# Kernel tuning notes

Hardware: AMD Instinct MI355X
Metric: run time of the kernel (lower is better)

The kernel has to match this reference:

```python
import jax, jax.numpy as jnp
import numpy as np

B, S, H, NH = 4, 1024, 2048, 32
HD = H // NH
EPS = 1e-5

def layer_norm(x, w, b):
    mu = jnp.mean(x, axis=-1, keepdims=True)
    var = jnp.mean(jnp.square(x - mu), axis=-1, keepdims=True)
    return (x - mu) * jax.lax.rsqrt(var + EPS) * w + b

def setup_inputs() -> dict:
    key = jax.random.key(0)
    ks = jax.random.split(key, 8)
    s = 0.02
    inp = {
        'hidden_states': jax.random.normal(ks[0], (B, S, H), jnp.float32),
        'mask': jnp.tril(jnp.ones((S, S), jnp.float32))[None, None],  # causal 0/1
        'ln1_w': jnp.ones((H,), jnp.float32), 'ln1_b': jnp.zeros((H,), jnp.float32),
        'w_qkv': s * jax.random.normal(ks[1], (H, 3 * H), jnp.float32),
        'b_qkv': jnp.zeros((3 * H,), jnp.float32),
        'w_dense': s * jax.random.normal(ks[2], (H, H), jnp.float32),
        'b_dense': jnp.zeros((H,), jnp.float32),
        'ln3_w': jnp.ones((H,), jnp.float32), 'ln3_b': jnp.zeros((H,), jnp.float32),
        'ln2_w': jnp.ones((H,), jnp.float32), 'ln2_b': jnp.zeros((H,), jnp.float32),
        'w_h4h': s * jax.random.normal(ks[3], (H, 4 * H), jnp.float32),
        'b_h4h': jnp.zeros((4 * H,), jnp.float32),
        'w_4hh': s * jax.random.normal(ks[4], (4 * H, H), jnp.float32),
        'b_4hh': jnp.zeros((H,), jnp.float32),
        'ln4_w': jnp.ones((H,), jnp.float32), 'ln4_b': jnp.zeros((H,), jnp.float32),
    }
    return inp

def _layer(hidden_states, mask, ln1_w, ln1_b, w_qkv, b_qkv, w_dense, b_dense,
           ln3_w, ln3_b, ln2_w, ln2_b, w_h4h, b_h4h, w_4hh, b_4hh, ln4_w, ln4_b):
    # --- input LN ---
    x1 = layer_norm(hidden_states, ln1_w, ln1_b)
    # --- self attention ---
    qkv = x1 @ w_qkv + b_qkv                              # [B,S,3H]
    q, k, v = jnp.split(qkv, 3, axis=-1)
    def heads(t):  # [B,S,H] -> [B,NH,S,HD]
        return t.reshape(B, S, NH, HD).transpose(0, 2, 1, 3)
    q, k, v = heads(q), heads(k), heads(v)
    scores = jnp.einsum('bnqd,bnkd->bnqk', q / jnp.sqrt(jnp.float32(HD)), k)
    scores = scores * mask - 10000.0 * (1.0 - mask)
    probs = jax.nn.softmax(scores, axis=-1)
    ctx = jnp.einsum('bnqk,bnkd->bnqd', probs, v)
    ctx = ctx.transpose(0, 2, 1, 3).reshape(B, S, H)
    attn_out = ctx @ w_dense + b_dense
    # sandwich LN on attention output
    attn_out = layer_norm(attn_out, ln3_w, ln3_b)
    ln_input = hidden_states + attn_out
    # --- MLP ---
    x2 = layer_norm(ln_input, ln2_w, ln2_b)
    inter = jax.nn.gelu(x2 @ w_h4h + b_h4h, approximate=True)
    mlp_out = inter @ w_4hh + b_4hh
    mlp_out = layer_norm(mlp_out, ln4_w, ln4_b)
    return ln_input + mlp_out

def reference(hidden_states, mask, ln1_w, ln1_b, w_qkv, b_qkv, w_dense, b_dense,
              ln3_w, ln3_b, ln2_w, ln2_b, w_h4h, b_h4h, w_4hh, b_4hh, ln4_w, ln4_b):
    return _layer(hidden_states, mask, ln1_w, ln1_b, w_qkv, b_qkv, w_dense, b_dense,
                  ln3_w, ln3_b, ln2_w, ln2_b, w_h4h, b_h4h, w_4hh, b_4hh, ln4_w, ln4_b)
```

## Files before the change

### kernel.cpp

```cpp
#include <hip/hip_runtime.h>
#include <cstdint>
#include <cstddef>

typedef __bf16 bf16_t;
typedef __bf16 bf16x8 __attribute__((ext_vector_type(8)));
typedef float f32x4 __attribute__((ext_vector_type(4)));

#define BB 4
#define SS 1024
#define HH 2048
#define NHH 32
#define HDD 64
#define MTOK 4096
#define QKVLD 6144

static constexpr size_t OFF_WQKV   = 0;
static constexpr size_t OFF_WDENSE = 25165824;
static constexpr size_t OFF_WH4H   = 33554432;
static constexpr size_t OFF_W4HH   = 67108864;
static constexpr size_t OFF_X1     = 100663296;
static constexpr size_t OFF_QKV    = 117440512;
static constexpr size_t OFF_ATTND2 = 150994944;
static constexpr size_t OFF_VT     = 167772160;
static constexpr size_t OFF_LNIN   = 184549376;
static constexpr size_t OFF_MLP    = 218103808;
static constexpr size_t OFF_MLP2   = 234881024;

__device__ __forceinline__ uint16_t f2bfu(float f) {
  union { float f; uint32_t u; } v; v.f = f;
  return (uint16_t)((v.u + 0x7FFFu + ((v.u >> 16) & 1u)) >> 16);
}
__device__ __forceinline__ bf16_t f2bf(float f) {
  union { uint16_t u; bf16_t b; } o; o.u = f2bfu(f);
  return o.b;
}
__device__ __forceinline__ float bfu2f(uint16_t u) {
  union { uint32_t u; float f; } v; v.u = ((uint32_t)u) << 16;
  return v.f;
}

__device__ __forceinline__ void g2l16(const void* g, void* l) {
  __builtin_amdgcn_global_load_lds(
      (const __attribute__((address_space(1))) void*)g,
      (__attribute__((address_space(3))) void*)l, 16, 0, 0);
}

__global__ void convert_all_kernel(const float* __restrict__ w0, bf16_t* __restrict__ o0,
                                   const float* __restrict__ w1, bf16_t* __restrict__ o1,
                                   const float* __restrict__ w2, bf16_t* __restrict__ o2,
                                   const float* __restrict__ w3, bf16_t* __restrict__ o3) {
  __shared__ float t[32][33];
  int id = blockIdx.x;
  const float* W; bf16_t* WT; int K, N, nt, idx;
  if (id < 12288)      { W = w0; WT = o0; K = 2048; N = 6144; nt = 192; idx = id; }
  else if (id < 16384) { W = w1; WT = o1; K = 2048; N = 2048; nt = 64;  idx = id - 12288; }
  else if (id < 32768) { W = w2; WT = o2; K = 2048; N = 8192; nt = 256; idx = id - 16384; }
  else                 { W = w3; WT = o3; K = 8192; N = 2048; nt = 64;  idx = id - 32768; }
  const int n0 = (idx % nt) * 32;
  const int k0 = (idx / nt) * 32;
  const int tx = threadIdx.x, ty = threadIdx.y;
#pragma unroll
  for (int j = 0; j < 4; ++j)
    t[ty + j * 8][tx] = W[(size_t)(k0 + ty + j * 8) * N + n0 + tx];
  __syncthreads();
#pragma unroll
  for (int j = 0; j < 4; ++j)
    WT[(size_t)(n0 + ty + j * 8) * K + k0 + tx] = f2bf(t[tx][ty + j * 8]);
}

__global__ void transpose_v_kernel(const bf16_t* __restrict__ qkv, bf16_t* __restrict__ vT) {
  __shared__ bf16_t t[32][33];
  const int s0 = blockIdx.x * 32;
  const int d0 = blockIdx.y * 32;
  const int bh = blockIdx.z;
  const int b = bh >> 5, h = bh & 31;
  const int tx = threadIdx.x, ty = threadIdx.y;
  const bf16_t* src = qkv + (size_t)b * SS * QKVLD + 2 * HH + h * HDD;
#pragma unroll
  for (int j = 0; j < 4; ++j)
    t[ty + j * 8][tx] = src[(size_t)(s0 + ty + j * 8) * QKVLD + d0 + tx];
  __syncthreads();
  bf16_t* dst = vT + (size_t)bh * HDD * SS;
#pragma unroll
  for (int j = 0; j < 4; ++j)
    dst[(size_t)(d0 + ty + j * 8) * SS + s0 + tx] = t[tx][ty + j * 8];
}

__device__ __forceinline__ void block_reduce2(float& s, float& ss) {
#pragma unroll
  for (int o = 32; o > 0; o >>= 1) {
    s += __shfl_down(s, o, 64);
    ss += __shfl_down(ss, o, 64);
  }
  __shared__ float red[8];
  const int wave = threadIdx.x >> 6;
  const int lane = threadIdx.x & 63;
  if (lane == 0) { red[wave] = s; red[4 + wave] = ss; }
  __syncthreads();
  s = red[0] + red[1] + red[2] + red[3];
  ss = red[4] + red[5] + red[6] + red[7];
  __syncthreads();
}

__device__ __forceinline__ void load8(const float* base, int tid, float* v) {
  float4 a = ((const float4*)base)[tid];
  float4 b = ((const float4*)base)[tid + 256];
  v[0] = a.x; v[1] = a.y; v[2] = a.z; v[3] = a.w;
  v[4] = b.x; v[5] = b.y; v[6] = b.z; v[7] = b.w;
}
__device__ __forceinline__ void load8bf(const bf16_t* base, int tid, float* v) {
  ushort4 a = ((const ushort4*)base)[tid];
  ushort4 b = ((const ushort4*)base)[tid + 256];
  v[0] = bfu2f(a.x); v[1] = bfu2f(a.y); v[2] = bfu2f(a.z); v[3] = bfu2f(a.w);
  v[4] = bfu2f(b.x); v[5] = bfu2f(b.y); v[6] = bfu2f(b.z); v[7] = bfu2f(b.w);
}
__device__ __forceinline__ void store8f(float* base, int tid, const float* v) {
  ((float4*)base)[tid] = make_float4(v[0], v[1], v[2], v[3]);
  ((float4*)base)[tid + 256] = make_float4(v[4], v[5], v[6], v[7]);
}
__device__ __forceinline__ void store8bf(bf16_t* base, int tid, const float* v) {
  ushort4 o0 = {f2bfu(v[0]), f2bfu(v[1]), f2bfu(v[2]), f2bfu(v[3])};
  ushort4 o1 = {f2bfu(v[4]), f2bfu(v[5]), f2bfu(v[6]), f2bfu(v[7])};
  ((ushort4*)base)[tid] = o0;
  ((ushort4*)base)[tid + 256] = o1;
}
__device__ __forceinline__ void row_stats(const float* v, float& mean, float& inv) {
  float s = 0.f, ss = 0.f;
#pragma unroll
  for (int i = 0; i < 8; ++i) { s += v[i]; ss += v[i] * v[i]; }
  block_reduce2(s, ss);
  mean = s * (1.0f / 2048.0f);
  float var = ss * (1.0f / 2048.0f) - mean * mean;
  inv = rsqrtf(var + 1e-5f);
}

__global__ __launch_bounds__(256) void ln1_kernel(const float* __restrict__ x,
                                                  const float* __restrict__ w,
                                                  const float* __restrict__ b,
                                                  bf16_t* __restrict__ out) {
  const int row = blockIdx.x, tid = threadIdx.x;
  float v[8], wv[8], bv[8], o[8];
  load8(x + (size_t)row * HH, tid, v);
  float mean, inv;
  row_stats(v, mean, inv);
  load8(w, tid, wv);
  load8(b, tid, bv);
#pragma unroll
  for (int i = 0; i < 8; ++i) o[i] = (v[i] - mean) * inv * wv[i] + bv[i];
  store8bf(out + (size_t)row * HH, tid, o);
}

__global__ __launch_bounds__(256) void fuse_mid_kernel(
    const bf16_t* __restrict__ ad, const bf16_t* __restrict__ ad2,
    const float* __restrict__ hid,
    const float* __restrict__ w3, const float* __restrict__ b3,
    const float* __restrict__ w2, const float* __restrict__ b2,
    float* __restrict__ lnin, bf16_t* __restrict__ x2) {
  const int row = blockIdx.x, tid = threadIdx.x;
  float a[8], a2[8], h[8], wv[8], bv[8], l[8], o[8];
  load8bf(ad + (size_t)row * HH, tid, a);
  load8bf(ad2 + (size_t)row * HH, tid, a2);
#pragma unroll
  for (int i = 0; i < 8; ++i) a[i] += a2[i];
  float mean3, inv3;
  row_stats(a, mean3, inv3);
  load8(hid + (size_t)row * HH, tid, h);
  load8(w3, tid, wv);
  load8(b3, tid, bv);
#pragma unroll
  for (int i = 0; i < 8; ++i) l[i] = h[i] + (a[i] - mean3) * inv3 * wv[i] + bv[i];
  store8f(lnin + (size_t)row * HH, tid, l);
  float mean2, inv2;
  row_stats(l, mean2, inv2);
  load8(w2, tid, wv);
  load8(b2, tid, bv);
#pragma unroll
  for (int i = 0; i < 8; ++i) o[i] = (l[i] - mean2) * inv2 * wv[i] + bv[i];
  store8bf(x2 + (size_t)row * HH, tid, o);
}

__global__ __launch_bounds__(256) void fuse_out_kernel(
    const bf16_t* __restrict__ mlp, const bf16_t* __restrict__ mlp2,
    const float* __restrict__ lnin,
    const float* __restrict__ w4, const float* __restrict__ b4,
    float* __restrict__ out) {
  const int row = blockIdx.x, tid = threadIdx.x;
  float m[8], m2[8], l[8], wv[8], bv[8], o[8];
  load8bf(mlp + (size_t)row * HH, tid, m);
  load8bf(mlp2 + (size_t)row * HH, tid, m2);
#pragma unroll
  for (int i = 0; i < 8; ++i) m[i] += m2[i];
  float mean4, inv4;
  row_stats(m, mean4, inv4);
  load8(lnin + (size_t)row * HH, tid, l);
  load8(w4, tid, wv);
  load8(b4, tid, bv);
#pragma unroll
  for (int i = 0; i < 8; ++i) o[i] = l[i] + (m[i] - mean4) * inv4 * wv[i] + bv[i];
  store8f(out + (size_t)row * HH, tid, o);
}

#define MFMA16(a, b, cc) __builtin_amdgcn_mfma_f32_16x16x32_bf16(a, b, cc, 0, 0, 0)

#define STAGE(ISB, BUF, HALF, KT) do {                                              \
    const char* _s = ((ISB) ? bS : aS) + (size_t)(HALF) * h128 + (size_t)(KT) * 128; \
    char* _d = lds + ((ISB) ? 65536 : 0) + (BUF) * 32768 + (HALF) * 16384 +         \
               wave * 1024;                                                         \
    g2l16(_s, _d);                                                                  \
    g2l16(_s + h64, _d + 8192);                                                     \
  } while (0)

#define LDA(BUF, MQ)                                                                \
  _Pragma("unroll") for (int mf = 0; mf < 4; ++mf) {                                \
    const char* _p = aRd + (BUF) * 32768 + (MQ) * 8192 + mf * 2048;                 \
    aR[mf * 2]     = *(const bf16x8*)(_p + colK0);                                  \
    aR[mf * 2 + 1] = *(const bf16x8*)(_p + colK1);                                  \
  }

#define LDB(BR, BUF, NQ)                                                            \
  _Pragma("unroll") for (int nf = 0; nf < 2; ++nf) {                                \
    const char* _p = bRd + (BUF) * 32768 + (NQ) * 4096 + nf * 2048;                 \
    BR[nf * 2]     = *(const bf16x8*)(_p + colK0);                                  \
    BR[nf * 2 + 1] = *(const bf16x8*)(_p + colK1);                                  \
  }

#define MMA(MQ, NQ, BR)                                                             \
  _Pragma("unroll") for (int mf = 0; mf < 4; ++mf)                                  \
  _Pragma("unroll") for (int nf = 0; nf < 2; ++nf)                                  \
  _Pragma("unroll") for (int ks = 0; ks < 2; ++ks)                                  \
    acc[(MQ) * 4 + mf][(NQ) * 2 + nf] =                                             \
        MFMA16(aR[mf * 2 + ks], BR[nf * 2 + ks], acc[(MQ) * 4 + mf][(NQ) * 2 + nf]);

#define BARS()                                                                      \
  __builtin_amdgcn_sched_barrier(0);                                                \
  __builtin_amdgcn_s_barrier();                                                     \
  asm volatile("s_waitcnt lgkmcnt(0)" ::: "memory");                                \
  __builtin_amdgcn_sched_barrier(0);                                                \
  __builtin_amdgcn_s_setprio(1);

#define ENDP()                                                                      \
  __builtin_amdgcn_s_setprio(0);                                                    \
  __builtin_amdgcn_sched_barrier(0);                                                \
  __builtin_amdgcn_s_barrier();

template <int EPI, int SPLITK>
__global__ __launch_bounds__(512, 2) void gemm256(
    const bf16_t* __restrict__ A, const bf16_t* __restrict__ BT,
    const float* __restrict__ bias, void* __restrict__ out0, void* __restrict__ out1,
    const int M, const int N, const int Keff, const int ldK) {
  __shared__ alignas(16) char lds[131072];
  const int tid = threadIdx.x;
  const int wave = tid >> 6, lane = tid & 63;
  const int wm = wave >> 2, wn = wave & 3;
  const int c = lane & 15, g = lane >> 4;

  const int nwg = gridDim.x;
  int bid = (blockIdx.x & 7) * (nwg >> 3) + (blockIdx.x >> 3);
  const int nm = M >> 8;
  int slice = 0;
  if (SPLITK == 2) {
    const int per = nm * (N >> 8);
    slice = bid >= per;
    bid -= slice * per;
  }
  const int mt = bid % nm, nt = bid / nm;

  const size_t ldb = (size_t)ldK * 2;
  const size_t h64 = (size_t)64 * ldb;
  const size_t h128 = 2 * h64;
  const char* aPan = (const char*)A + (size_t)(mt * 256) * ldb + (size_t)(slice * Keff) * 2;
  const char* bPan = (const char*)BT + (size_t)(nt * 256) * ldb + (size_t)(slice * Keff) * 2;

  const int srow = tid >> 3;
  const int scb = ((tid & 7) << 4) ^ ((srow & 7) << 4);
  const char* aS = aPan + (size_t)srow * ldb + scb;
  const char* bS = bPan + (size_t)srow * ldb + scb;

  const int x4 = (c & 7) << 4;
  const int colK0 = (g * 16) ^ x4;
  const int colK1 = (64 + g * 16) ^ x4;
  const char* aRd = lds + wm * 16384 + c * 128;
  const char* bRd = lds + 65536 + (wn >> 1) * 16384 + ((wn & 1) * 64 + c) * 128;

  f32x4 acc[8][4] = {};
  bf16x8 aR[8], b0R[4], b1R[4];

  const int NITER = Keff >> 7;
  const int NT2 = NITER * 2;

  STAGE(1, 0, 0, 0); STAGE(1, 0, 1, 0); STAGE(0, 0, 0, 0); STAGE(0, 0, 1, 0);
  STAGE(1, 1, 0, 1); STAGE(1, 1, 1, 1);
  asm volatile("s_waitcnt vmcnt(4)" ::: "memory");
  __builtin_amdgcn_s_barrier();

  for (int it = 0; it < NITER; ++it) {
    const int ktb = 2 * it + 1;
    int kt2 = 2 * it + 2; if (kt2 >= NT2) kt2 = 0;
    int kt3 = 2 * it + 3; if (kt3 >= NT2) kt3 = 0;
    LDA(0, 0); LDB(b0R, 0, 0); STAGE(0, 1, 0, ktb);
    BARS(); MMA(0, 0, b0R); ENDP();
    LDB(b1R, 0, 1); STAGE(0, 1, 1, ktb);
    BARS(); MMA(0, 1, b1R); ENDP();
    LDA(0, 1); STAGE(1, 0, 0, kt2);
    BARS(); MMA(1, 1, b1R); ENDP();
    STAGE(1, 0, 1, kt2);
    asm volatile("s_waitcnt vmcnt(4)" ::: "memory");
    BARS(); MMA(1, 0, b0R); ENDP();
    LDA(1, 0); LDB(b0R, 1, 0); STAGE(0, 0, 0, kt2);
    BARS(); MMA(0, 0, b0R); ENDP();
    LDB(b1R, 1, 1); STAGE(0, 0, 1, kt2);
    BARS(); MMA(0, 1, b1R); ENDP();
    LDA(1, 1); STAGE(1, 1, 0, kt3);
    BARS(); MMA(1, 1, b1R); ENDP();
    STAGE(1, 1, 1, kt3);
    asm volatile("s_waitcnt vmcnt(4)" ::: "memory");
    BARS(); MMA(1, 0, b0R); ENDP();
  }

  const int rowb = mt * 256 + wm * 128 + g * 4;
  const int colb = nt * 256 + wn * 64 + c;
  if constexpr (EPI == 0) {
    bf16_t* o = (bf16_t*)(slice ? out1 : out0);
    float bvv[4];
#pragma unroll
    for (int nf = 0; nf < 4; ++nf) bvv[nf] = (slice == 0) ? bias[colb + nf * 16] : 0.0f;
#pragma unroll
    for (int mf = 0; mf < 8; ++mf) {
      const int r = rowb + mf * 16;
#pragma unroll
      for (int e = 0; e < 4; ++e) {
        bf16_t* orow = o + (size_t)(r + e) * N + colb;
#pragma unroll
        for (int nf = 0; nf < 4; ++nf)
          orow[nf * 16] = f2bf(acc[mf][nf][e] + bvv[nf]);
      }
    }
  } else if constexpr (EPI == 1) {
    bf16_t* o = (bf16_t*)out0;
    float bvv[4];
#pragma unroll
    for (int nf = 0; nf < 4; ++nf) bvv[nf] = bias[colb + nf * 16];
#pragma unroll
    for (int mf = 0; mf < 8; ++mf) {
      const int r = rowb + mf * 16;
#pragma unroll
      for (int e = 0; e < 4; ++e) {
        bf16_t* orow = o + (size_t)(r + e) * N + colb;
#pragma unroll
        for (int nf = 0; nf < 4; ++nf)
          orow[nf * 16] = f2bf(acc[mf][nf][e] + bvv[nf]);
      }
    }
  } else {
    bf16_t* o = (bf16_t*)out0;
    float bvv[4];
#pragma unroll
    for (int nf = 0; nf < 4; ++nf) bvv[nf] = bias[colb + nf * 16];
#pragma unroll
    for (int mf = 0; mf < 8; ++mf) {
      const int r = rowb + mf * 16;
#pragma unroll
      for (int e = 0; e < 4; ++e) {
        bf16_t* orow = o + (size_t)(r + e) * N + colb;
#pragma unroll
        for (int nf = 0; nf < 4; ++nf) {
          float u = acc[mf][nf][e] + bvv[nf];
          float cc2 = 0.7978845608f * (u + 0.044715f * u * u * u);
          float ex = __expf(2.0f * cc2);
          float th = 1.0f - 2.0f / (ex + 1.0f);
          orow[nf * 16] = f2bf(0.5f * u * (1.0f + th));
        }
      }
    }
  }
}

__global__ __launch_bounds__(512) void attn_kernel(
    const bf16_t* __restrict__ qkv, const bf16_t* __restrict__ vT,
    bf16_t* __restrict__ ctx) {
  __shared__ alignas(16) char Ksm[8192];
  __shared__ alignas(16) char Vsm[8192];
  __shared__ alignas(16) char Psm[16384];

  const int id = blockIdx.x;
  const int qt = 7 - (id >> 7);
  const int bh = id & 127;
  const int b = bh >> 5, h = bh & 31;
  const int tid = threadIdx.x;
  const int wave = tid >> 6;
  const int lane = tid & 63;
  const int q0 = qt * 128;
  const int q0w = q0 + wave * 16;
  const int c = lane & 15;
  const int g = lane >> 4;

  const bf16_t* qb = qkv + ((size_t)b * SS + q0w) * QKVLD + h * HDD;
  const bf16x8 qa0 = *(const bf16x8*)(qb + (size_t)c * QKVLD + g * 8);
  const bf16x8 qa1 = *(const bf16x8*)(qb + (size_t)c * QKVLD + 32 + g * 8);

  f32x4 o[4] = {};
  float mrow[4], lrow[4];
#pragma unroll
  for (int e = 0; e < 4; ++e) { mrow[e] = -1e30f; lrow[e] = 0.0f; }

  const int sr = tid >> 3;
  const int sgb = ((tid & 7) * 16) ^ ((sr & 7) << 4);
  const char* kgb = (const char*)(qkv + (size_t)b * SS * QKVLD + HH + h * HDD);
  const char* vgb = (const char*)(vT + (size_t)bh * HDD * SS);
  char* kdst = Ksm + wave * 1024;
  char* vdst = Vsm + wave * 1024;
  char* Pw = Psm + wave * 2048;

  const int ntiles = (q0 + 128) >> 6;

  for (int t = 0; t < ntiles; ++t) {
    const int kb = t * 64;
    g2l16(kgb + (size_t)(kb + sr) * (QKVLD * 2) + sgb, kdst);
    g2l16(vgb + (size_t)sr * 2048 + (size_t)kb * 2 + sgb, vdst);
    __syncthreads();

    if (kb < q0w + 16) {
      f32x4 s[4] = {};
#pragma unroll
      for (int sub = 0; sub < 4; ++sub) {
        const int n = sub * 16 + c;
        const int x = (n & 7) << 4;
        bf16x8 kf0 = *(const bf16x8*)(Ksm + n * 128 + ((g * 16) ^ x));
        bf16x8 kf1 = *(const bf16x8*)(Ksm + n * 128 + ((64 + g * 16) ^ x));
        s[sub] = MFMA16(qa0, kf0, s[sub]);
        s[sub] = MFMA16(qa1, kf1, s[sub]);
      }
      const bool diag = (kb + 63 > q0w);
      float pv[4][4];
#pragma unroll
      for (int sub = 0; sub < 4; ++sub)
#pragma unroll
        for (int e = 0; e < 4; ++e) {
          float sv = s[sub][e] * 0.125f;
          if (diag && (kb + sub * 16 + c > q0w + g * 4 + e)) sv = -10000.0f;
          pv[sub][e] = sv;
        }
      float scale[4];
#pragma unroll
      for (int e = 0; e < 4; ++e) {
        float mx = fmaxf(fmaxf(pv[0][e], pv[1][e]), fmaxf(pv[2][e], pv[3][e]));
        mx = fmaxf(mx, __shfl_xor(mx, 1, 64));
        mx = fmaxf(mx, __shfl_xor(mx, 2, 64));
        mx = fmaxf(mx, __shfl_xor(mx, 4, 64));
        mx = fmaxf(mx, __shfl_xor(mx, 8, 64));
        const float mnew = fmaxf(mrow[e], mx);
        scale[e] = __expf(mrow[e] - mnew);
        mrow[e] = mnew;
      }
#pragma unroll
      for (int e = 0; e < 4; ++e) {
        const int row = g * 4 + e;
        const int xr = (row & 7) << 4;
        float sum = 0.0f;
#pragma unroll
        for (int sub = 0; sub < 4; ++sub) {
          float p = __expf(pv[sub][e] - mrow[e]);
          sum += p;
          const int cb = (sub * 16 + c) * 2;
          *(bf16_t*)(Pw + row * 128 + (cb ^ xr)) = f2bf(p);
        }
        sum += __shfl_xor(sum, 1, 64);
        sum += __shfl_xor(sum, 2, 64);
        sum += __shfl_xor(sum, 4, 64);
        sum += __shfl_xor(sum, 8, 64);
        lrow[e] = lrow[e] * scale[e] + sum;
      }
#pragma unroll
      for (int d = 0; d < 4; ++d)
#pragma unroll
        for (int e = 0; e < 4; ++e) o[d][e] *= scale[e];
      const int xa = (c & 7) << 4;
      bf16x8 pa0 = *(const bf16x8*)(Pw + c * 128 + ((g * 16) ^ xa));
      bf16x8 pa1 = *(const bf16x8*)(Pw + c * 128 + ((64 + g * 16) ^ xa));
#pragma unroll
      for (int d = 0; d < 4; ++d) {
        const int n = d * 16 + c;
        const int xv = (n & 7) << 4;
        bf16x8 vf0 = *(const bf16x8*)(Vsm + n * 128 + ((g * 16) ^ xv));
        bf16x8 vf1 = *(const bf16x8*)(Vsm + n * 128 + ((64 + g * 16) ^ xv));
        o[d] = MFMA16(pa0, vf0, o[d]);
        o[d] = MFMA16(pa1, vf1, o[d]);
      }
    }
    __syncthreads();
  }

#pragma unroll
  for (int e = 0; e < 4; ++e) {
    const int qrow = q0w + g * 4 + e;
    const float inv = 1.0f / lrow[e];
#pragma unroll
    for (int d = 0; d < 4; ++d)
      ctx[((size_t)b * SS + qrow) * HH + h * 64 + d * 16 + c] = f2bf(o[d][e] * inv);
  }
}

extern "C" void kernel_launch(void* const* d_in, const int* in_sizes, int n_in,
                              void* d_out, int out_size, void* d_ws, size_t ws_size,
                              hipStream_t stream) {
  const float* hidden = (const float*)d_in[0];
  const float* ln1w = (const float*)d_in[2];
  const float* ln1b = (const float*)d_in[3];
  const float* wqkv = (const float*)d_in[4];
  const float* bqkv = (const float*)d_in[5];
  const float* wdense = (const float*)d_in[6];
  const float* bdense = (const float*)d_in[7];
  const float* ln3w = (const float*)d_in[8];
  const float* ln3b = (const float*)d_in[9];
  const float* ln2w = (const float*)d_in[10];
  const float* ln2b = (const float*)d_in[11];
  const float* wh4h = (const float*)d_in[12];
  const float* bh4h = (const float*)d_in[13];
  const float* w4hh = (const float*)d_in[14];
  const float* b4hh = (const float*)d_in[15];
  const float* ln4w = (const float*)d_in[16];
  const float* ln4b = (const float*)d_in[17];

  char* ws = (char*)d_ws;
  bf16_t* wqkvT = (bf16_t*)(ws + OFF_WQKV);
  bf16_t* wdenseT = (bf16_t*)(ws + OFF_WDENSE);
  bf16_t* wh4hT = (bf16_t*)(ws + OFF_WH4H);
  bf16_t* w4hhT = (bf16_t*)(ws + OFF_W4HH);
  bf16_t* x1 = (bf16_t*)(ws + OFF_X1);
  bf16_t* qkv = (bf16_t*)(ws + OFF_QKV);
  bf16_t* vT = (bf16_t*)(ws + OFF_VT);
  bf16_t* ctx = (bf16_t*)(ws + OFF_X1);
  bf16_t* attnd = (bf16_t*)(ws + OFF_QKV);
  bf16_t* attnd2 = (bf16_t*)(ws + OFF_ATTND2);
  float* lnin = (float*)(ws + OFF_LNIN);
  bf16_t* x2 = (bf16_t*)(ws + OFF_X1);
  bf16_t* inter = (bf16_t*)(ws + OFF_QKV);
  bf16_t* mlp = (bf16_t*)(ws + OFF_MLP);
  bf16_t* mlp2 = (bf16_t*)(ws + OFF_MLP2);

  dim3 tb(32, 8);
  convert_all_kernel<<<dim3(49152), tb, 0, stream>>>(wqkv, wqkvT, wdense, wdenseT,
                                                     wh4h, wh4hT, w4hh, w4hhT);

  ln1_kernel<<<MTOK, 256, 0, stream>>>(hidden, ln1w, ln1b, x1);

  gemm256<1, 1><<<dim3((6144 / 256) * (4096 / 256)), 512, 0, stream>>>(
      x1, wqkvT, bqkv, (void*)qkv, nullptr, MTOK, 6144, 2048, 2048);

  transpose_v_kernel<<<dim3(SS / 32, HDD / 32, BB * NHH), tb, 0, stream>>>(qkv, vT);

  attn_kernel<<<dim3(1024), 512, 0, stream>>>(qkv, vT, ctx);

  gemm256<0, 2><<<dim3((2048 / 256) * (4096 / 256) * 2), 512, 0, stream>>>(
      ctx, wdenseT, bdense, (void*)attnd, (void*)attnd2, MTOK, 2048, 1024, 2048);

  fuse_mid_kernel<<<MTOK, 256, 0, stream>>>(attnd, attnd2, hidden, ln3w, ln3b, ln2w, ln2b, lnin, x2);

  gemm256<2, 1><<<dim3((8192 / 256) * (4096 / 256)), 512, 0, stream>>>(
      x2, wh4hT, bh4h, (void*)inter, nullptr, MTOK, 8192, 2048, 2048);

  gemm256<0, 2><<<dim3((2048 / 256) * (4096 / 256) * 2), 512, 0, stream>>>(
      inter, w4hhT, b4hh, (void*)mlp, (void*)mlp2, MTOK, 2048, 4096, 8192);

  fuse_out_kernel<<<MTOK, 256, 0, stream>>>(mlp, mlp2, lnin, ln4w, ln4b, (float*)d_out);
}
```

Baseline: 594.3 us.

## Software-pipeline LDS fragment loads behind MFMA phases in GEMM main loop

Restructures the 256x256 GEMM K-loop so that the LDS-to-register fragment loads for the next phase are issued after the current phase's MFMAs, between the priority drop and the closing barrier. A prologue load before the loop and a final load at the end of each iteration keep the pipeline primed. The explicit lgkmcnt(0) waits and sched_barrier fences are removed, leaving wait placement and interleaving to the compiler. The goal is to hide LDS read latency under matrix-core work. The cost is more live fragment registers and reliance on the compiler to order LDS reads correctly against the async global-to-LDS staging.

```diff
diff --git a/kernel.cpp b/kernel.cpp
--- a/kernel.cpp
+++ b/kernel.cpp
@@ -231,16 +231,14 @@
     acc[(MQ) * 4 + mf][(NQ) * 2 + nf] =                                             \
         MFMA16(aR[mf * 2 + ks], BR[nf * 2 + ks], acc[(MQ) * 4 + mf][(NQ) * 2 + nf]);
 
-#define BARS()                                                                      \
-  __builtin_amdgcn_sched_barrier(0);                                                \
+#define PH_BEGIN()                                                                  \
   __builtin_amdgcn_s_barrier();                                                     \
-  asm volatile("s_waitcnt lgkmcnt(0)" ::: "memory");                                \
-  __builtin_amdgcn_sched_barrier(0);                                                \
   __builtin_amdgcn_s_setprio(1);
 
-#define ENDP()                                                                      \
-  __builtin_amdgcn_s_setprio(0);                                                    \
-  __builtin_amdgcn_sched_barrier(0);                                                \
+#define PH_MID()                                                                    \
+  __builtin_amdgcn_s_setprio(0);
+
+#define PH_END()                                                                    \
   __builtin_amdgcn_s_barrier();
 
 template <int EPI, int SPLITK>
@@ -292,29 +290,45 @@
   STAGE(1, 1, 0, 1); STAGE(1, 1, 1, 1);
   asm volatile("s_waitcnt vmcnt(4)" ::: "memory");
   __builtin_amdgcn_s_barrier();
+  LDA(0, 0);
+  LDB(b0R, 0, 0);
 
   for (int it = 0; it < NITER; ++it) {
     const int ktb = 2 * it + 1;
     int kt2 = 2 * it + 2; if (kt2 >= NT2) kt2 = 0;
     int kt3 = 2 * it + 3; if (kt3 >= NT2) kt3 = 0;
-    LDA(0, 0); LDB(b0R, 0, 0); STAGE(0, 1, 0, ktb);
-    BARS(); MMA(0, 0, b0R); ENDP();
-    LDB(b1R, 0, 1); STAGE(0, 1, 1, ktb);
-    BARS(); MMA(0, 1, b1R); ENDP();
-    LDA(0, 1); STAGE(1, 0, 0, kt2);
-    BARS(); MMA(1, 1, b1R); ENDP();
+    STAGE(0, 1, 0, ktb);
+    PH_BEGIN(); MMA(0, 0, b0R); PH_MID();
+    LDB(b1R, 0, 1);
+    PH_END();
+    STAGE(0, 1, 1, ktb);
+    PH_BEGIN(); MMA(0, 1, b1R); PH_MID();
+    LDA(0, 1);
+    PH_END();
+    STAGE(1, 0, 0, kt2);
+    PH_BEGIN(); MMA(1, 1, b1R); PH_MID();
+    PH_END();
     STAGE(1, 0, 1, kt2);
     asm volatile("s_waitcnt vmcnt(4)" ::: "memory");
-    BARS(); MMA(1, 0, b0R); ENDP();
-    LDA(1, 0); LDB(b0R, 1, 0); STAGE(0, 0, 0, kt2);
-    BARS(); MMA(0, 0, b0R); ENDP();
-    LDB(b1R, 1, 1); STAGE(0, 0, 1, kt2);
-    BARS(); MMA(0, 1, b1R); ENDP();
-    LDA(1, 1); STAGE(1, 1, 0, kt3);
-    BARS(); MMA(1, 1, b1R); ENDP();
+    PH_BEGIN(); MMA(1, 0, b0R); PH_MID();
+    LDA(1, 0); LDB(b0R, 1, 0);
+    PH_END();
+    STAGE(0, 0, 0, kt2);
+    PH_BEGIN(); MMA(0, 0, b0R); PH_MID();
+    LDB(b1R, 1, 1);
+    PH_END();
+    STAGE(0, 0, 1, kt2);
+    PH_BEGIN(); MMA(0, 1, b1R); PH_MID();
+    LDA(1, 1);
+    PH_END();
+    STAGE(1, 1, 0, kt3);
+    PH_BEGIN(); MMA(1, 1, b1R); PH_MID();
+    PH_END();
     STAGE(1, 1, 1, kt3);
     asm volatile("s_waitcnt vmcnt(4)" ::: "memory");
-    BARS(); MMA(1, 0, b0R); ENDP();
+    PH_BEGIN(); MMA(1, 0, b0R); PH_MID();
+    LDA(0, 0); LDB(b0R, 0, 0);
+    PH_END();
   }
 
   const int rowb = mt * 256 + wm * 128 + g * 4;
```

New measurement: 592.7 us. Within noise of the previous version (-0.3%).
